# Kernel optimization log

Hardware: AMD Instinct MI355X
Metric: run time of the kernel (lower is better)

The kernel has to match this reference:

```python
import jax, jax.numpy as jnp
import numpy as np

N_NODES = 100000
N_EDGES = 3200000
IN_CH = 24
HIDDEN = 64
N_CLASSES = 16


def _sage_conv(x, src, dst, W_l, b_l, W_r, num_nodes):
    # mean-aggregate neighbor features at destination nodes
    msg = x[src]                                             # [E, F] gather
    agg = jax.ops.segment_sum(msg, dst, num_segments=num_nodes)
    deg = jax.ops.segment_sum(jnp.ones((src.shape[0],), x.dtype), dst,
                              num_segments=num_nodes)
    mean = agg / jnp.maximum(deg, 1.0)[:, None]
    # PyG SAGEConv: lin_l(aggregated) + lin_r(self); bias lives in lin_l
    return mean @ W_l.T + b_l + x @ W_r.T


def setup_inputs() -> dict:
    key = jax.random.key(0)
    ks = jax.random.split(key, 8)
    x = jax.random.normal(ks[0], (N_NODES, IN_CH), dtype=jnp.float32)
    edge_index = jax.random.randint(ks[1], (2, N_EDGES), 0, N_NODES, dtype=jnp.int64)
    s1 = 1.0 / np.sqrt(IN_CH)
    s2 = 1.0 / np.sqrt(HIDDEN)
    return {
        "x": x,
        "edge_index": edge_index,
        "W1_l": jax.random.normal(ks[2], (HIDDEN, IN_CH), dtype=jnp.float32) * s1,
        "b1": jnp.zeros((HIDDEN,), jnp.float32),
        "W1_r": jax.random.normal(ks[3], (HIDDEN, IN_CH), dtype=jnp.float32) * s1,
        "W2_l": jax.random.normal(ks[4], (HIDDEN, HIDDEN), dtype=jnp.float32) * s2,
        "b2": jnp.zeros((HIDDEN,), jnp.float32),
        "W2_r": jax.random.normal(ks[5], (HIDDEN, HIDDEN), dtype=jnp.float32) * s2,
        "Wc": jax.random.normal(ks[6], (N_CLASSES, HIDDEN), dtype=jnp.float32) * s2,
        "bc": jnp.zeros((N_CLASSES,), jnp.float32),
    }


def reference(x, edge_index, W1_l, b1, W1_r, W2_l, b2, W2_r, Wc, bc):
    num_nodes = x.shape[0]
    src, dst = edge_index[0], edge_index[1]
    h = _sage_conv(x, src, dst, W1_l, b1, W1_r, num_nodes)
    h = jax.nn.relu(h)
    # dropout is identity in eval mode
    embeddings = _sage_conv(h, src, dst, W2_l, b2, W2_r, num_nodes)
    logits = embeddings @ Wc.T + bc
    return (logits, embeddings)
```

## Files before the change

kernel.cpp:

```cpp
#include <hip/hip_runtime.h>

#define N_NODES 100000
#define N_EDGES 3200000
#define IN_CH 24
#define HIDDEN 64
#define N_CLASSES 16

#define NBUCK 782
#define CAP 4608
#define PTBLOCKS 256
#define PTCHUNK 12500
#define NSTRIPS (N_NODES / 16)

typedef __attribute__((ext_vector_type(8))) short short8;
typedef __attribute__((ext_vector_type(4))) float float4_;
typedef __attribute__((ext_vector_type(2))) float float2v;
typedef __attribute__((ext_vector_type(4))) int int4v;
typedef __attribute__((ext_vector_type(2))) unsigned uint2v;

__device__ unsigned llvm_amdgcn_raw_buffer_load_u32(int4v, int, int, int) __asm("llvm.amdgcn.raw.buffer.load.i32");
__device__ uint2v llvm_amdgcn_raw_buffer_load_u32x2(int4v, int, int, int) __asm("llvm.amdgcn.raw.buffer.load.v2i32");

__device__ __forceinline__ int4v make_srd(const void* p, unsigned bytes) {
    unsigned long long a = (unsigned long long)p;
    int4v r;
    r.x = (int)(unsigned)a;
    r.y = (int)((unsigned)(a >> 32) & 0xFFFFu);
    r.z = (int)bytes;
    r.w = 0x00020000;
    return r;
}

__device__ __forceinline__ unsigned short f2bf(float f) {
    union { float f; unsigned int u; } v; v.f = f;
    unsigned int u = v.u;
    return (unsigned short)((u + 0x7FFFu + ((u >> 16) & 1u)) >> 16);
}
__device__ __forceinline__ unsigned cvt_pk_bf16(float a, float b) {
    unsigned r;
    asm("v_cvt_pk_bf16_f32 %0, %1, %2" : "=v"(r) : "v"(a), "v"(b));
    return r;
}
__device__ __forceinline__ unsigned short pk_fp8(float a, float b) {
    return (unsigned short)(__builtin_amdgcn_cvt_pk_fp8_f32(a, b, 0, false) & 0xFFFF);
}
__device__ __forceinline__ void accum_dw(float2v* A, unsigned w) {
    A[0] += __builtin_amdgcn_cvt_pk_f32_fp8(w, false);
    A[1] += __builtin_amdgcn_cvt_pk_f32_fp8(w, true);
}


__global__ __launch_bounds__(256) void k_prep(const float* __restrict__ W1l,
                                              const float* __restrict__ W1r,
                                              const float* __restrict__ W2l,
                                              const float* __restrict__ W2r,
                                              const float* __restrict__ Wc,
                                              const float* __restrict__ b2,
                                              const float* __restrict__ bc,
                                              unsigned short* __restrict__ Bt1,
                                              unsigned short* __restrict__ Bt2,
                                              float* __restrict__ bias2,
                                              int* __restrict__ bucketFill) {
    int t = threadIdx.x;
    for (int i = t; i < NBUCK; i += 256) bucketFill[i] = 0;
    for (int i = t; i < 64 * 64; i += 256) {
        int o = i >> 6, k = i & 63;
        float v = (k < 24) ? W1r[o * 24 + k] : ((k < 48) ? W1l[o * 24 + k - 24] : 0.f);
        Bt1[i] = f2bf(v);
    }
    for (int i = t; i < 64 * 128; i += 256) {
        int o = i >> 7, k = i & 127;
        float v = (k < 64) ? W2l[o * 64 + k] : W2r[o * 64 + k - 64];
        Bt2[i] = f2bf(v);
    }
    for (int i = t; i < 16 * 128; i += 256) {
        int c = i >> 7, k = i & 127;
        const float* M = (k < 64) ? W2l : W2r;
        int kk = k & 63;
        float s = 0.f;
        for (int j = 0; j < 64; j++) s += Wc[c * 64 + j] * M[j * 64 + kk];
        Bt2[(64 + c) * 128 + k] = f2bf(s);
    }
    for (int i = t; i < 80; i += 256) {
        if (i < 64) bias2[i] = b2[i];
        else {
            int c = i - 64;
            float s = bc[c];
            for (int j = 0; j < 64; j++) s += Wc[c * 64 + j] * b2[j];
            bias2[i] = s;
        }
    }
}


__global__ __launch_bounds__(1024) void k_part(const int* __restrict__ src,
                                               const int* __restrict__ dst,
                                               int* __restrict__ bucketFill,
                                               unsigned int* __restrict__ pedges) {
    __shared__ int cntL[NBUCK];
    __shared__ int baseL[NBUCK];
    int t = threadIdx.x;
    int cbeg = blockIdx.x * PTCHUNK;
    int d[13], s[13];
#pragma unroll
    for (int k = 0; k < 13; k++) {
        int o = k * 1024 + t;
        bool ok = o < PTCHUNK;
        d[k] = ok ? dst[cbeg + o] : -1;
        s[k] = ok ? src[cbeg + o] : 0;
    }
    for (int i = t; i < NBUCK; i += 1024) cntL[i] = 0;
    __syncthreads();
#pragma unroll
    for (int k = 0; k < 13; k++)
        if (d[k] >= 0) atomicAdd(&cntL[d[k] >> 7], 1);
    __syncthreads();
    for (int i = t; i < NBUCK; i += 1024) {
        int c = cntL[i];
        if (c) baseL[i] = i * CAP + atomicAdd(&bucketFill[i], c);
        cntL[i] = 0;
    }
    __syncthreads();
#pragma unroll
    for (int k = 0; k < 13; k++)
        if (d[k] >= 0) {
            int bk = d[k] >> 7;
            int r = atomicAdd(&cntL[bk], 1);
            pedges[baseL[bk] + r] = ((unsigned int)(d[k] & 127) << 17) | (unsigned int)s[k];
        }
}

__global__ __launch_bounds__(1024) void k_bucket(const unsigned int* __restrict__ pedges,
                                                 const int* __restrict__ bucketFill,
                                                 int2* __restrict__ begend,
                                                 int* __restrict__ srcs, int N) {
    __shared__ int ncnt[128];
    __shared__ int sps[128];
    int b = blockIdx.x;
    int t = threadIdx.x;
    int eb0 = b * CAP;
    int m = bucketFill[b];
    unsigned int v[5];
#pragma unroll
    for (int k = 0; k < 5; k++) {
        int o = k * 1024 + t;
        v[k] = (o < m) ? pedges[eb0 + o] : 0xFFFFFFFFu;
    }
    if (t < 128) ncnt[t] = 0;
    __syncthreads();
#pragma unroll
    for (int k = 0; k < 5; k++)
        if (v[k] != 0xFFFFFFFFu) atomicAdd(&ncnt[v[k] >> 17], 1);
    __syncthreads();
    int myc = (t < 128) ? ncnt[t] : 0;
    int val = myc;
    if (t < 128) sps[t] = val;
    __syncthreads();
    for (int off = 1; off < 128; off <<= 1) {
        int vv = (t >= off && t < 128) ? sps[t - off] : 0;
        __syncthreads();
        if (t < 128) { val += vv; sps[t] = val; }
        __syncthreads();
    }
    int mybase = val - myc;
    int node = b * 128 + t;
    if (t < 128 && node < N) {
        int2 be; be.x = eb0 + mybase; be.y = eb0 + mybase + myc;
        begend[node] = be;
    }
    if (t < 128) { sps[t] = mybase; ncnt[t] = 0; }
    if (t < 32) srcs[eb0 + m + t] = 0;
    __syncthreads();
#pragma unroll
    for (int k = 0; k < 5; k++)
        if (v[k] != 0xFFFFFFFFu) {
            unsigned int nl = v[k] >> 17;
            int r = atomicAdd(&ncnt[nl], 1);
            srcs[eb0 + sps[nl] + r] = (int)(v[k] & 0x1FFFF);
        }
}

__global__ __launch_bounds__(256) void k_castx(const float* __restrict__ x,
                                               unsigned int* __restrict__ A1u,
                                               unsigned short* __restrict__ X8s) {
    int gid = blockIdx.x * 256 + threadIdx.x;
    if (gid >= N_NODES * 16) return;
    int n = gid >> 4, kp = gid & 15;
    if (kp < 12) {
        const float2 v = *(const float2*)(x + n * 24 + kp * 2);
        A1u[n * 32 + kp] = (unsigned int)f2bf(v.x) | ((unsigned int)f2bf(v.y) << 16);
        X8s[n * 16 + kp] = pk_fp8(v.x, v.y);
    } else {
        int p = kp - 12;
        uint2 z; z.x = 0u; z.y = 0u;
        *(uint2*)(A1u + n * 32 + 24 + p * 2) = z;
        X8s[n * 16 + kp] = 0;
    }
}


__global__ __launch_bounds__(256) void k_agg1(const unsigned int* __restrict__ X8u,
                                              const int2* __restrict__ begend,
                                              const int* __restrict__ srcs,
                                              unsigned int* __restrict__ A1w, int N) {
    int node = (blockIdx.x * 256 + threadIdx.x) >> 6;
    int lane = threadIdx.x & 63;
    if (node >= N) return;
    int2 be = begend[node];
    int b = be.x, e = be.y;
    int grp = lane >> 3;
    int sub = lane & 7;
    const int4v srdX = make_srd(X8u, N_NODES * 32u);
    const int4v srdS = make_srd(srcs, (unsigned)NBUCK * CAP * 4u);
    int suboff = sub * 4;
    float2v A[2] = {{0.f, 0.f}, {0.f, 0.f}};
    int nfull = (e - b) & ~31;
    int j = b;
    int vo = (b + grp) * 4;
    for (; j < b + nfull; j += 32, vo += 128) {
        int s0 = (int)llvm_amdgcn_raw_buffer_load_u32(srdS, vo, 0, 0);
        int s1 = (int)llvm_amdgcn_raw_buffer_load_u32(srdS, vo + 32, 0, 0);
        int s2 = (int)llvm_amdgcn_raw_buffer_load_u32(srdS, vo + 64, 0, 0);
        int s3 = (int)llvm_amdgcn_raw_buffer_load_u32(srdS, vo + 96, 0, 0);
        unsigned u0 = llvm_amdgcn_raw_buffer_load_u32(srdX, (s0 << 5) + suboff, 0, 0);
        unsigned u1 = llvm_amdgcn_raw_buffer_load_u32(srdX, (s1 << 5) + suboff, 0, 0);
        unsigned u2 = llvm_amdgcn_raw_buffer_load_u32(srdX, (s2 << 5) + suboff, 0, 0);
        unsigned u3 = llvm_amdgcn_raw_buffer_load_u32(srdX, (s3 << 5) + suboff, 0, 0);
        accum_dw(A, u0); accum_dw(A, u1); accum_dw(A, u2); accum_dw(A, u3);
    }
    if (j < e) {
        int j0 = j + grp;
        int s0 = (int)llvm_amdgcn_raw_buffer_load_u32(srdS, vo, 0, 0);
        int s1 = (int)llvm_amdgcn_raw_buffer_load_u32(srdS, vo + 32, 0, 0);
        int s2 = (int)llvm_amdgcn_raw_buffer_load_u32(srdS, vo + 64, 0, 0);
        int s3 = (int)llvm_amdgcn_raw_buffer_load_u32(srdS, vo + 96, 0, 0);
        int o0 = (j0 < e)      ? ((s0 << 5) + suboff) : 0x7FFF0000;
        int o1 = (j0 + 8 < e)  ? ((s1 << 5) + suboff) : 0x7FFF0000;
        int o2 = (j0 + 16 < e) ? ((s2 << 5) + suboff) : 0x7FFF0000;
        int o3 = (j0 + 24 < e) ? ((s3 << 5) + suboff) : 0x7FFF0000;
        unsigned u0 = llvm_amdgcn_raw_buffer_load_u32(srdX, o0, 0, 0);
        unsigned u1 = llvm_amdgcn_raw_buffer_load_u32(srdX, o1, 0, 0);
        unsigned u2 = llvm_amdgcn_raw_buffer_load_u32(srdX, o2, 0, 0);
        unsigned u3 = llvm_amdgcn_raw_buffer_load_u32(srdX, o3, 0, 0);
        accum_dw(A, u0); accum_dw(A, u1); accum_dw(A, u2); accum_dw(A, u3);
    }
#pragma unroll
    for (int mm = 8; mm <= 32; mm <<= 1) {
#pragma unroll
        for (int q = 0; q < 2; q++) {
            float2v t;
            t.x = __shfl_xor(A[q].x, mm, 64);
            t.y = __shfl_xor(A[q].y, mm, 64);
            A[q] += t;
        }
    }
    if (lane < 8) {
        float inv = __builtin_amdgcn_rcpf((float)max(e - b, 1));
        uint2v o;
        o.x = cvt_pk_bf16(A[0].x * inv, A[0].y * inv);
        o.y = cvt_pk_bf16(A[1].x * inv, A[1].y * inv);
        *(uint2v*)(A1w + (size_t)node * 32 + 12 + sub * 2) = o;
    }
}

__global__ __launch_bounds__(256) void k_agg2(const unsigned int* __restrict__ H8u,
                                              const int2* __restrict__ begend,
                                              const int* __restrict__ srcs,
                                              unsigned int* __restrict__ A2w, int N) {
    int node = (blockIdx.x * 256 + threadIdx.x) >> 6;
    int lane = threadIdx.x & 63;
    if (node >= N) return;
    int2 be = begend[node];
    int b = be.x, e = be.y;
    int grp = lane >> 3;
    int sub = lane & 7;
    const int4v srdH = make_srd(H8u, N_NODES * 64u);
    const int4v srdS = make_srd(srcs, (unsigned)NBUCK * CAP * 4u);
    int suboff = sub * 8;
    float2v A[4] = {{0.f, 0.f}, {0.f, 0.f}, {0.f, 0.f}, {0.f, 0.f}};
    int nfull = (e - b) & ~31;
    int j = b;
    int vo = (b + grp) * 4;
    for (; j < b + nfull; j += 32, vo += 128) {
        int s0 = (int)llvm_amdgcn_raw_buffer_load_u32(srdS, vo, 0, 0);
        int s1 = (int)llvm_amdgcn_raw_buffer_load_u32(srdS, vo + 32, 0, 0);
        int s2 = (int)llvm_amdgcn_raw_buffer_load_u32(srdS, vo + 64, 0, 0);
        int s3 = (int)llvm_amdgcn_raw_buffer_load_u32(srdS, vo + 96, 0, 0);
        uint2v u0 = llvm_amdgcn_raw_buffer_load_u32x2(srdH, (s0 << 6) + suboff, 0, 0);
        uint2v u1 = llvm_amdgcn_raw_buffer_load_u32x2(srdH, (s1 << 6) + suboff, 0, 0);
        uint2v u2 = llvm_amdgcn_raw_buffer_load_u32x2(srdH, (s2 << 6) + suboff, 0, 0);
        uint2v u3 = llvm_amdgcn_raw_buffer_load_u32x2(srdH, (s3 << 6) + suboff, 0, 0);
        accum_dw(A, u0.x); accum_dw(A + 2, u0.y);
        accum_dw(A, u1.x); accum_dw(A + 2, u1.y);
        accum_dw(A, u2.x); accum_dw(A + 2, u2.y);
        accum_dw(A, u3.x); accum_dw(A + 2, u3.y);
    }
    if (j < e) {
        int j0 = j + grp;
        int s0 = (int)llvm_amdgcn_raw_buffer_load_u32(srdS, vo, 0, 0);
        int s1 = (int)llvm_amdgcn_raw_buffer_load_u32(srdS, vo + 32, 0, 0);
        int s2 = (int)llvm_amdgcn_raw_buffer_load_u32(srdS, vo + 64, 0, 0);
        int s3 = (int)llvm_amdgcn_raw_buffer_load_u32(srdS, vo + 96, 0, 0);
        int o0 = (j0 < e)      ? ((s0 << 6) + suboff) : 0x7FFF0000;
        int o1 = (j0 + 8 < e)  ? ((s1 << 6) + suboff) : 0x7FFF0000;
        int o2 = (j0 + 16 < e) ? ((s2 << 6) + suboff) : 0x7FFF0000;
        int o3 = (j0 + 24 < e) ? ((s3 << 6) + suboff) : 0x7FFF0000;
        uint2v u0 = llvm_amdgcn_raw_buffer_load_u32x2(srdH, o0, 0, 0);
        uint2v u1 = llvm_amdgcn_raw_buffer_load_u32x2(srdH, o1, 0, 0);
        uint2v u2 = llvm_amdgcn_raw_buffer_load_u32x2(srdH, o2, 0, 0);
        uint2v u3 = llvm_amdgcn_raw_buffer_load_u32x2(srdH, o3, 0, 0);
        accum_dw(A, u0.x); accum_dw(A + 2, u0.y);
        accum_dw(A, u1.x); accum_dw(A + 2, u1.y);
        accum_dw(A, u2.x); accum_dw(A + 2, u2.y);
        accum_dw(A, u3.x); accum_dw(A + 2, u3.y);
    }
#pragma unroll
    for (int mm = 8; mm <= 32; mm <<= 1) {
#pragma unroll
        for (int q = 0; q < 4; q++) {
            float2v t;
            t.x = __shfl_xor(A[q].x, mm, 64);
            t.y = __shfl_xor(A[q].y, mm, 64);
            A[q] += t;
        }
    }
    if (lane < 8) {
        float inv = __builtin_amdgcn_rcpf((float)max(e - b, 1));
        uint4 o;
        o.x = cvt_pk_bf16(A[0].x * inv, A[0].y * inv);
        o.y = cvt_pk_bf16(A[1].x * inv, A[1].y * inv);
        o.z = cvt_pk_bf16(A[2].x * inv, A[2].y * inv);
        o.w = cvt_pk_bf16(A[3].x * inv, A[3].y * inv);
        *(uint4*)(A2w + (size_t)node * 64 + sub * 4) = o;
    }
}


__global__ __launch_bounds__(256) void k_gemm1(const unsigned short* __restrict__ A1,
                                               const unsigned short* __restrict__ Bt1,
                                               const float* __restrict__ b1,
                                               unsigned short* __restrict__ A2s,
                                               unsigned char* __restrict__ H8b) {
    int wave = (blockIdx.x * 256 + threadIdx.x) >> 6;
    int lane = threadIdx.x & 63;
    int m = lane & 15, quad = lane >> 4;
    if (wave >= NSTRIPS) return;
    short8 bf[4][2];
#pragma unroll
    for (int t = 0; t < 4; t++)
#pragma unroll
        for (int s = 0; s < 2; s++)
            bf[t][s] = *(const short8*)(Bt1 + (t * 16 + m) * 64 + s * 32 + quad * 8);
    float bias[4];
#pragma unroll
    for (int t = 0; t < 4; t++) bias[t] = b1[t * 16 + m];

    int row0 = wave * 16;
    short8 a0 = *(const short8*)(A1 + (row0 + m) * 64 + quad * 8);
    short8 a1 = *(const short8*)(A1 + (row0 + m) * 64 + 32 + quad * 8);
    float4_ acc[4];
#pragma unroll
    for (int t = 0; t < 4; t++) {
        float4_ c = {0.f, 0.f, 0.f, 0.f};
        c = __builtin_amdgcn_mfma_f32_16x16x32_bf16(a0, bf[t][0], c, 0, 0, 0);
        c = __builtin_amdgcn_mfma_f32_16x16x32_bf16(a1, bf[t][1], c, 0, 0, 0);
        acc[t] = c;
    }
#pragma unroll
    for (int t = 0; t < 4; t++) {
        int col = t * 16 + m;
#pragma unroll
        for (int r = 0; r < 4; r++) {
            int row = row0 + quad * 4 + r;
            float v = fmaxf(acc[t][r] + bias[t], 0.f);
            A2s[row * 128 + 64 + col] = f2bf(v);
            H8b[row * 64 + col] =
                (unsigned char)(__builtin_amdgcn_cvt_pk_fp8_f32(v, 0.f, 0, false) & 0xFF);
        }
    }
}

__global__ __launch_bounds__(256) void k_gemm2(const unsigned short* __restrict__ Bt2,
                                               const float* __restrict__ bias2,
                                               unsigned short* A2s,
                                               float* logits) {
    int wave = (blockIdx.x * 256 + threadIdx.x) >> 6;
    int lane = threadIdx.x & 63;
    int m = lane & 15, quad = lane >> 4;
    if (wave >= NSTRIPS) return;
    short8 bf[5][4];
#pragma unroll
    for (int t = 0; t < 5; t++)
#pragma unroll
        for (int s = 0; s < 4; s++)
            bf[t][s] = *(const short8*)(Bt2 + (t * 16 + m) * 128 + s * 32 + quad * 8);
    float bias[5];
#pragma unroll
    for (int t = 0; t < 5; t++) bias[t] = bias2[t * 16 + m];

    int row0 = wave * 16;
    short8 a[4];
#pragma unroll
    for (int s = 0; s < 4; s++)
        a[s] = *(const short8*)(A2s + (row0 + m) * 128 + s * 32 + quad * 8);
    float4_ acc[5];
#pragma unroll
    for (int t = 0; t < 5; t++) {
        float4_ c = {0.f, 0.f, 0.f, 0.f};
#pragma unroll
        for (int s = 0; s < 4; s++)
            c = __builtin_amdgcn_mfma_f32_16x16x32_bf16(a[s], bf[t][s], c, 0, 0, 0);
        acc[t] = c;
    }
    float* embp = (float*)A2s;
#pragma unroll
    for (int t = 0; t < 4; t++) {
#pragma unroll
        for (int r = 0; r < 4; r++) {
            int row = row0 + quad * 4 + r;
            embp[row * 64 + t * 16 + m] = acc[t][r] + bias[t];
        }
    }
#pragma unroll
    for (int r = 0; r < 4; r++) {
        int row = row0 + quad * 4 + r;
        logits[row * 16 + m] = acc[4][r] + bias[4];
    }
}


extern "C" void kernel_launch(void* const* d_in, const int* in_sizes, int n_in,
                              void* d_out, int out_size, void* d_ws, size_t ws_size,
                              hipStream_t stream) {
    const float* x = (const float*)d_in[0];
    const int* edge = (const int*)d_in[1];
    const int* srcIdx = edge;
    const int* dstIdx = edge + N_EDGES;
    const float* W1l = (const float*)d_in[2];
    const float* b1  = (const float*)d_in[3];
    const float* W1r = (const float*)d_in[4];
    const float* W2l = (const float*)d_in[5];
    const float* b2  = (const float*)d_in[6];
    const float* W2r = (const float*)d_in[7];
    const float* Wc  = (const float*)d_in[8];
    const float* bc  = (const float*)d_in[9];

    float* logits = (float*)d_out;
    unsigned short* A2s = (unsigned short*)((float*)d_out + (size_t)N_NODES * N_CLASSES);
    unsigned int* A2u = (unsigned int*)A2s;

    char* w = (char*)d_ws;
    auto carve = [&](size_t bytes) {
        char* p = w;
        w += (bytes + 255) & ~(size_t)255;
        return p;
    };
    int2* begend         = (int2*)carve((size_t)N_NODES * sizeof(int2));
    int* srcs            = (int*)carve((size_t)NBUCK * CAP * sizeof(int));
    unsigned int* A1u    = (unsigned int*)carve((size_t)N_NODES * 32 * sizeof(unsigned int));
    unsigned short* X8s  = (unsigned short*)carve((size_t)N_NODES * 32);
    unsigned char* H8b   = (unsigned char*)carve((size_t)N_NODES * 64);
    int* bucketFill      = (int*)carve(NBUCK * sizeof(int));
    unsigned short* Bt1  = (unsigned short*)carve(64 * 64 * sizeof(unsigned short));
    unsigned short* Bt2  = (unsigned short*)carve(80 * 128 * sizeof(unsigned short));
    float* bias2         = (float*)carve(80 * sizeof(float));

    unsigned int* pedges = (unsigned int*)A1u;
    unsigned short* A1s = (unsigned short*)A1u;
    unsigned int* X8u = (unsigned int*)X8s;
    unsigned int* H8u = (unsigned int*)H8b;

    k_prep<<<1, 256, 0, stream>>>(W1l, W1r, W2l, W2r, Wc, b2, bc, Bt1, Bt2, bias2,
                                  bucketFill);
    k_part<<<PTBLOCKS, 1024, 0, stream>>>(srcIdx, dstIdx, bucketFill, pedges);
    k_bucket<<<NBUCK, 1024, 0, stream>>>(pedges, bucketFill, begend, srcs, N_NODES);

    k_castx<<<(N_NODES * 16 + 255) / 256, 256, 0, stream>>>(x, A1u, X8s);
    int agrid = (N_NODES * 64 + 255) / 256;
    k_agg1<<<agrid, 256, 0, stream>>>(X8u, begend, srcs, A1u, N_NODES);
    k_gemm1<<<(NSTRIPS + 3) / 4, 256, 0, stream>>>(A1s, Bt1, b1, A2s, H8b);
    k_agg2<<<agrid, 256, 0, stream>>>(H8u, begend, srcs, A2u, N_NODES);
    k_gemm2<<<(NSTRIPS + 3) / 4, 256, 0, stream>>>(Bt2, bias2, A2s, logits);
}
```

Measured before the change: 278.2 us.

## Split layer-2 aggregation into two feature-half passes

Splits the second-layer neighbor aggregation into two kernel launches, each gathering only half of every 64-byte H row (32 bytes) per edge. The goal is a smaller gather working set per pass, so the half-feature table stays better resident in cache during random-source gathers. In exchange the edge index list and begin/end ranges are read twice, there is one extra launch, and each gather becomes a narrower 4-byte load.

```diff
diff --git a/kernel.cpp b/kernel.cpp
--- a/kernel.cpp
+++ b/kernel.cpp
@@ -263,10 +263,11 @@
     }
 }
 
-__global__ __launch_bounds__(256) void k_agg2(const unsigned int* __restrict__ H8u,
-                                              const int2* __restrict__ begend,
-                                              const int* __restrict__ srcs,
-                                              unsigned int* __restrict__ A2w, int N) {
+template <int HALF>
+__global__ __launch_bounds__(256) void k_agg2h(const unsigned int* __restrict__ H8u,
+                                               const int2* __restrict__ begend,
+                                               const int* __restrict__ srcs,
+                                               unsigned int* __restrict__ A2w, int N) {
     int node = (blockIdx.x * 256 + threadIdx.x) >> 6;
     int lane = threadIdx.x & 63;
     if (node >= N) return;
@@ -276,8 +277,8 @@
     int sub = lane & 7;
     const int4v srdH = make_srd(H8u, N_NODES * 64u);
     const int4v srdS = make_srd(srcs, (unsigned)NBUCK * CAP * 4u);
-    int suboff = sub * 8;
-    float2v A[4] = {{0.f, 0.f}, {0.f, 0.f}, {0.f, 0.f}, {0.f, 0.f}};
+    int suboff = HALF * 32 + sub * 4;
+    float2v A[2] = {{0.f, 0.f}, {0.f, 0.f}};
     int nfull = (e - b) & ~31;
     int j = b;
     int vo = (b + grp) * 4;
@@ -286,14 +287,11 @@
         int s1 = (int)llvm_amdgcn_raw_buffer_load_u32(srdS, vo + 32, 0, 0);
         int s2 = (int)llvm_amdgcn_raw_buffer_load_u32(srdS, vo + 64, 0, 0);
         int s3 = (int)llvm_amdgcn_raw_buffer_load_u32(srdS, vo + 96, 0, 0);
-        uint2v u0 = llvm_amdgcn_raw_buffer_load_u32x2(srdH, (s0 << 6) + suboff, 0, 0);
-        uint2v u1 = llvm_amdgcn_raw_buffer_load_u32x2(srdH, (s1 << 6) + suboff, 0, 0);
-        uint2v u2 = llvm_amdgcn_raw_buffer_load_u32x2(srdH, (s2 << 6) + suboff, 0, 0);
-        uint2v u3 = llvm_amdgcn_raw_buffer_load_u32x2(srdH, (s3 << 6) + suboff, 0, 0);
-        accum_dw(A, u0.x); accum_dw(A + 2, u0.y);
-        accum_dw(A, u1.x); accum_dw(A + 2, u1.y);
-        accum_dw(A, u2.x); accum_dw(A + 2, u2.y);
-        accum_dw(A, u3.x); accum_dw(A + 2, u3.y);
+        unsigned u0 = llvm_amdgcn_raw_buffer_load_u32(srdH, (s0 << 6) + suboff, 0, 0);
+        unsigned u1 = llvm_amdgcn_raw_buffer_load_u32(srdH, (s1 << 6) + suboff, 0, 0);
+        unsigned u2 = llvm_amdgcn_raw_buffer_load_u32(srdH, (s2 << 6) + suboff, 0, 0);
+        unsigned u3 = llvm_amdgcn_raw_buffer_load_u32(srdH, (s3 << 6) + suboff, 0, 0);
+        accum_dw(A, u0); accum_dw(A, u1); accum_dw(A, u2); accum_dw(A, u3);
     }
     if (j < e) {
         int j0 = j + grp;
@@ -305,19 +303,16 @@
         int o1 = (j0 + 8 < e)  ? ((s1 << 6) + suboff) : 0x7FFF0000;
         int o2 = (j0 + 16 < e) ? ((s2 << 6) + suboff) : 0x7FFF0000;
         int o3 = (j0 + 24 < e) ? ((s3 << 6) + suboff) : 0x7FFF0000;
-        uint2v u0 = llvm_amdgcn_raw_buffer_load_u32x2(srdH, o0, 0, 0);
-        uint2v u1 = llvm_amdgcn_raw_buffer_load_u32x2(srdH, o1, 0, 0);
-        uint2v u2 = llvm_amdgcn_raw_buffer_load_u32x2(srdH, o2, 0, 0);
-        uint2v u3 = llvm_amdgcn_raw_buffer_load_u32x2(srdH, o3, 0, 0);
-        accum_dw(A, u0.x); accum_dw(A + 2, u0.y);
-        accum_dw(A, u1.x); accum_dw(A + 2, u1.y);
-        accum_dw(A, u2.x); accum_dw(A + 2, u2.y);
-        accum_dw(A, u3.x); accum_dw(A + 2, u3.y);
+        unsigned u0 = llvm_amdgcn_raw_buffer_load_u32(srdH, o0, 0, 0);
+        unsigned u1 = llvm_amdgcn_raw_buffer_load_u32(srdH, o1, 0, 0);
+        unsigned u2 = llvm_amdgcn_raw_buffer_load_u32(srdH, o2, 0, 0);
+        unsigned u3 = llvm_amdgcn_raw_buffer_load_u32(srdH, o3, 0, 0);
+        accum_dw(A, u0); accum_dw(A, u1); accum_dw(A, u2); accum_dw(A, u3);
     }
 #pragma unroll
     for (int mm = 8; mm <= 32; mm <<= 1) {
 #pragma unroll
-        for (int q = 0; q < 4; q++) {
+        for (int q = 0; q < 2; q++) {
             float2v t;
             t.x = __shfl_xor(A[q].x, mm, 64);
             t.y = __shfl_xor(A[q].y, mm, 64);
@@ -326,12 +321,10 @@
     }
     if (lane < 8) {
         float inv = __builtin_amdgcn_rcpf((float)max(e - b, 1));
-        uint4 o;
+        uint2v o;
         o.x = cvt_pk_bf16(A[0].x * inv, A[0].y * inv);
         o.y = cvt_pk_bf16(A[1].x * inv, A[1].y * inv);
-        o.z = cvt_pk_bf16(A[2].x * inv, A[2].y * inv);
-        o.w = cvt_pk_bf16(A[3].x * inv, A[3].y * inv);
-        *(uint4*)(A2w + (size_t)node * 64 + sub * 4) = o;
+        *(uint2v*)(A2w + (size_t)node * 64 + HALF * 16 + sub * 2) = o;
     }
 }
 
@@ -479,6 +472,7 @@
     int agrid = (N_NODES * 64 + 255) / 256;
     k_agg1<<<agrid, 256, 0, stream>>>(X8u, begend, srcs, A1u, N_NODES);
     k_gemm1<<<(NSTRIPS + 3) / 4, 256, 0, stream>>>(A1s, Bt1, b1, A2s, H8b);
-    k_agg2<<<agrid, 256, 0, stream>>>(H8u, begend, srcs, A2u, N_NODES);
+    k_agg2h<0><<<agrid, 256, 0, stream>>>(H8u, begend, srcs, A2u, N_NODES);
+    k_agg2h<1><<<agrid, 256, 0, stream>>>(H8u, begend, srcs, A2u, N_NODES);
     k_gemm2<<<(NSTRIPS + 3) / 4, 256, 0, stream>>>(Bt2, bias2, A2s, logits);
 }
```

Result: slower. 304.2 us (+9.3%).

## Fuse neighbor aggregation with MFMA GEMM per 16-node tile in each layer

Applied to the files above, without the earlier changes.

Replaces the separate aggregate and GEMM kernels for both layers with fused kernels. Each block aggregates 16 nodes (4 per wave) into LDS and then runs the bf16 MFMA for that tile directly. Layer 1 now builds its self-feature operand straight from fp32 x, so the bf16 A1 staging buffer is no longer written or read, and k_castx only emits the fp8 copy. This removes global round trips of intermediates and two launches. In exchange each wave walks 4 nodes serially before the GEMM, which reduces gather parallelism per wave and adds a block barrier. The logits tile is computed only by wave 3, so that wave does extra work.

```diff
diff --git a/kernel.cpp b/kernel.cpp
--- a/kernel.cpp
+++ b/kernel.cpp
@@ -10,7 +10,6 @@
 #define CAP 4608
 #define PTBLOCKS 256
 #define PTCHUNK 12500
-#define NSTRIPS (N_NODES / 16)
 
 typedef __attribute__((ext_vector_type(8))) short short8;
 typedef __attribute__((ext_vector_type(4))) float float4_;
@@ -47,6 +46,11 @@
 __device__ __forceinline__ void accum_dw(float2v* A, unsigned w) {
     A[0] += __builtin_amdgcn_cvt_pk_f32_fp8(w, false);
     A[1] += __builtin_amdgcn_cvt_pk_f32_fp8(w, true);
+}
+__device__ __forceinline__ short8 mk8(unsigned d0, unsigned d1, unsigned d2, unsigned d3) {
+    union { unsigned u[4]; short8 s; } v;
+    v.u[0] = d0; v.u[1] = d1; v.u[2] = d2; v.u[3] = d3;
+    return v.s;
 }
 
 
@@ -181,250 +185,243 @@
 }
 
 __global__ __launch_bounds__(256) void k_castx(const float* __restrict__ x,
-                                               unsigned int* __restrict__ A1u,
                                                unsigned short* __restrict__ X8s) {
     int gid = blockIdx.x * 256 + threadIdx.x;
     if (gid >= N_NODES * 16) return;
     int n = gid >> 4, kp = gid & 15;
     if (kp < 12) {
         const float2 v = *(const float2*)(x + n * 24 + kp * 2);
-        A1u[n * 32 + kp] = (unsigned int)f2bf(v.x) | ((unsigned int)f2bf(v.y) << 16);
         X8s[n * 16 + kp] = pk_fp8(v.x, v.y);
     } else {
-        int p = kp - 12;
-        uint2 z; z.x = 0u; z.y = 0u;
-        *(uint2*)(A1u + n * 32 + 24 + p * 2) = z;
         X8s[n * 16 + kp] = 0;
     }
 }
 
 
-__global__ __launch_bounds__(256) void k_agg1(const unsigned int* __restrict__ X8u,
-                                              const int2* __restrict__ begend,
-                                              const int* __restrict__ srcs,
-                                              unsigned int* __restrict__ A1w, int N) {
-    int node = (blockIdx.x * 256 + threadIdx.x) >> 6;
+__global__ __launch_bounds__(256) void k_fuse1(const float* __restrict__ x,
+                                               const unsigned int* __restrict__ X8u,
+                                               const int2* __restrict__ begend,
+                                               const int* __restrict__ srcs,
+                                               const unsigned short* __restrict__ Bt1,
+                                               const float* __restrict__ b1,
+                                               unsigned short* __restrict__ A2s,
+                                               unsigned char* __restrict__ H8b) {
+    __shared__ unsigned int lds_mean[16][20];
+    int w = threadIdx.x >> 6;
     int lane = threadIdx.x & 63;
-    if (node >= N) return;
-    int2 be = begend[node];
-    int b = be.x, e = be.y;
+    int base = blockIdx.x * 16;
     int grp = lane >> 3;
     int sub = lane & 7;
     const int4v srdX = make_srd(X8u, N_NODES * 32u);
     const int4v srdS = make_srd(srcs, (unsigned)NBUCK * CAP * 4u);
     int suboff = sub * 4;
-    float2v A[2] = {{0.f, 0.f}, {0.f, 0.f}};
-    int nfull = (e - b) & ~31;
-    int j = b;
-    int vo = (b + grp) * 4;
-    for (; j < b + nfull; j += 32, vo += 128) {
-        int s0 = (int)llvm_amdgcn_raw_buffer_load_u32(srdS, vo, 0, 0);
-        int s1 = (int)llvm_amdgcn_raw_buffer_load_u32(srdS, vo + 32, 0, 0);
-        int s2 = (int)llvm_amdgcn_raw_buffer_load_u32(srdS, vo + 64, 0, 0);
-        int s3 = (int)llvm_amdgcn_raw_buffer_load_u32(srdS, vo + 96, 0, 0);
-        unsigned u0 = llvm_amdgcn_raw_buffer_load_u32(srdX, (s0 << 5) + suboff, 0, 0);
-        unsigned u1 = llvm_amdgcn_raw_buffer_load_u32(srdX, (s1 << 5) + suboff, 0, 0);
-        unsigned u2 = llvm_amdgcn_raw_buffer_load_u32(srdX, (s2 << 5) + suboff, 0, 0);
-        unsigned u3 = llvm_amdgcn_raw_buffer_load_u32(srdX, (s3 << 5) + suboff, 0, 0);
-        accum_dw(A, u0); accum_dw(A, u1); accum_dw(A, u2); accum_dw(A, u3);
-    }
-    if (j < e) {
-        int j0 = j + grp;
-        int s0 = (int)llvm_amdgcn_raw_buffer_load_u32(srdS, vo, 0, 0);
-        int s1 = (int)llvm_amdgcn_raw_buffer_load_u32(srdS, vo + 32, 0, 0);
-        int s2 = (int)llvm_amdgcn_raw_buffer_load_u32(srdS, vo + 64, 0, 0);
-        int s3 = (int)llvm_amdgcn_raw_buffer_load_u32(srdS, vo + 96, 0, 0);
-        int o0 = (j0 < e)      ? ((s0 << 5) + suboff) : 0x7FFF0000;
-        int o1 = (j0 + 8 < e)  ? ((s1 << 5) + suboff) : 0x7FFF0000;
-        int o2 = (j0 + 16 < e) ? ((s2 << 5) + suboff) : 0x7FFF0000;
-        int o3 = (j0 + 24 < e) ? ((s3 << 5) + suboff) : 0x7FFF0000;
-        unsigned u0 = llvm_amdgcn_raw_buffer_load_u32(srdX, o0, 0, 0);
-        unsigned u1 = llvm_amdgcn_raw_buffer_load_u32(srdX, o1, 0, 0);
-        unsigned u2 = llvm_amdgcn_raw_buffer_load_u32(srdX, o2, 0, 0);
-        unsigned u3 = llvm_amdgcn_raw_buffer_load_u32(srdX, o3, 0, 0);
-        accum_dw(A, u0); accum_dw(A, u1); accum_dw(A, u2); accum_dw(A, u3);
-    }
-#pragma unroll
-    for (int mm = 8; mm <= 32; mm <<= 1) {
-#pragma unroll
-        for (int q = 0; q < 2; q++) {
-            float2v t;
-            t.x = __shfl_xor(A[q].x, mm, 64);
-            t.y = __shfl_xor(A[q].y, mm, 64);
-            A[q] += t;
-        }
-    }
-    if (lane < 8) {
-        float inv = __builtin_amdgcn_rcpf((float)max(e - b, 1));
-        uint2v o;
-        o.x = cvt_pk_bf16(A[0].x * inv, A[0].y * inv);
-        o.y = cvt_pk_bf16(A[1].x * inv, A[1].y * inv);
-        *(uint2v*)(A1w + (size_t)node * 32 + 12 + sub * 2) = o;
-    }
-}
-
-__global__ __launch_bounds__(256) void k_agg2(const unsigned int* __restrict__ H8u,
-                                              const int2* __restrict__ begend,
-                                              const int* __restrict__ srcs,
-                                              unsigned int* __restrict__ A2w, int N) {
-    int node = (blockIdx.x * 256 + threadIdx.x) >> 6;
+
+    for (int i = 0; i < 4; i++) {
+        int il = w * 4 + i;
+        int2 be = begend[base + il];
+        int b = be.x, e = be.y;
+        float2v A[2] = {{0.f, 0.f}, {0.f, 0.f}};
+        int nfull = (e - b) & ~31;
+        int j = b;
+        int vo = (b + grp) * 4;
+        for (; j < b + nfull; j += 32, vo += 128) {
+            int s0 = (int)llvm_amdgcn_raw_buffer_load_u32(srdS, vo, 0, 0);
+            int s1 = (int)llvm_amdgcn_raw_buffer_load_u32(srdS, vo + 32, 0, 0);
+            int s2 = (int)llvm_amdgcn_raw_buffer_load_u32(srdS, vo + 64, 0, 0);
+            int s3 = (int)llvm_amdgcn_raw_buffer_load_u32(srdS, vo + 96, 0, 0);
+            unsigned u0 = llvm_amdgcn_raw_buffer_load_u32(srdX, (s0 << 5) + suboff, 0, 0);
+            unsigned u1 = llvm_amdgcn_raw_buffer_load_u32(srdX, (s1 << 5) + suboff, 0, 0);
+            unsigned u2 = llvm_amdgcn_raw_buffer_load_u32(srdX, (s2 << 5) + suboff, 0, 0);
+            unsigned u3 = llvm_amdgcn_raw_buffer_load_u32(srdX, (s3 << 5) + suboff, 0, 0);
+            accum_dw(A, u0); accum_dw(A, u1); accum_dw(A, u2); accum_dw(A, u3);
+        }
+        if (j < e) {
+            int j0 = j + grp;
+            int s0 = (int)llvm_amdgcn_raw_buffer_load_u32(srdS, vo, 0, 0);
+            int s1 = (int)llvm_amdgcn_raw_buffer_load_u32(srdS, vo + 32, 0, 0);
+            int s2 = (int)llvm_amdgcn_raw_buffer_load_u32(srdS, vo + 64, 0, 0);
+            int s3 = (int)llvm_amdgcn_raw_buffer_load_u32(srdS, vo + 96, 0, 0);
+            int o0 = (j0 < e)      ? ((s0 << 5) + suboff) : 0x7FFF0000;
+            int o1 = (j0 + 8 < e)  ? ((s1 << 5) + suboff) : 0x7FFF0000;
+            int o2 = (j0 + 16 < e) ? ((s2 << 5) + suboff) : 0x7FFF0000;
+            int o3 = (j0 + 24 < e) ? ((s3 << 5) + suboff) : 0x7FFF0000;
+            unsigned u0 = llvm_amdgcn_raw_buffer_load_u32(srdX, o0, 0, 0);
+            unsigned u1 = llvm_amdgcn_raw_buffer_load_u32(srdX, o1, 0, 0);
+            unsigned u2 = llvm_amdgcn_raw_buffer_load_u32(srdX, o2, 0, 0);
+            unsigned u3 = llvm_amdgcn_raw_buffer_load_u32(srdX, o3, 0, 0);
+            accum_dw(A, u0); accum_dw(A, u1); accum_dw(A, u2); accum_dw(A, u3);
+        }
+#pragma unroll
+        for (int mm = 8; mm <= 32; mm <<= 1) {
+#pragma unroll
+            for (int q = 0; q < 2; q++) {
+                float2v t;
+                t.x = __shfl_xor(A[q].x, mm, 64);
+                t.y = __shfl_xor(A[q].y, mm, 64);
+                A[q] += t;
+            }
+        }
+        if (lane < 8) {
+            float inv = __builtin_amdgcn_rcpf((float)max(e - b, 1));
+            lds_mean[il][sub * 2]     = cvt_pk_bf16(A[0].x * inv, A[0].y * inv);
+            lds_mean[il][sub * 2 + 1] = cvt_pk_bf16(A[1].x * inv, A[1].y * inv);
+        }
+    }
+    __syncthreads();
+
+    int m = lane & 15, quad = lane >> 4;
+    int row = base + m;
+    short8 bf0 = *(const short8*)(Bt1 + (w * 16 + m) * 64 + quad * 8);
+    short8 bf1 = *(const short8*)(Bt1 + (w * 16 + m) * 64 + 32 + quad * 8);
+    float bias = b1[w * 16 + m];
+    short8 a0, a1;
+    if (quad < 3) {
+        const float4* xp = (const float4*)(x + row * 24 + quad * 8);
+        float4 v0 = xp[0], v1 = xp[1];
+        a0 = mk8(cvt_pk_bf16(v0.x, v0.y), cvt_pk_bf16(v0.z, v0.w),
+                 cvt_pk_bf16(v1.x, v1.y), cvt_pk_bf16(v1.z, v1.w));
+    } else {
+        a0 = *(const short8*)&lds_mean[m][0];
+    }
+    if (quad == 0)      a1 = *(const short8*)&lds_mean[m][4];
+    else if (quad == 1) a1 = *(const short8*)&lds_mean[m][8];
+    else                a1 = mk8(0u, 0u, 0u, 0u);
+    float4_ c = {0.f, 0.f, 0.f, 0.f};
+    c = __builtin_amdgcn_mfma_f32_16x16x32_bf16(a0, bf0, c, 0, 0, 0);
+    c = __builtin_amdgcn_mfma_f32_16x16x32_bf16(a1, bf1, c, 0, 0, 0);
+    int col = w * 16 + m;
+#pragma unroll
+    for (int r = 0; r < 4; r++) {
+        int row2 = base + quad * 4 + r;
+        float v = fmaxf(c[r] + bias, 0.f);
+        A2s[row2 * 128 + 64 + col] = f2bf(v);
+        H8b[row2 * 64 + col] =
+            (unsigned char)(__builtin_amdgcn_cvt_pk_fp8_f32(v, 0.f, 0, false) & 0xFF);
+    }
+}
+
+__global__ __launch_bounds__(256) void k_fuse2(const unsigned int* __restrict__ H8u,
+                                               const int2* __restrict__ begend,
+                                               const int* __restrict__ srcs,
+                                               const unsigned short* __restrict__ Bt2,
+                                               const float* __restrict__ bias2,
+                                               unsigned short* A2s,
+                                               float* __restrict__ logits) {
+    __shared__ unsigned int lds_h[16][36];
+    int w = threadIdx.x >> 6;
     int lane = threadIdx.x & 63;
-    if (node >= N) return;
-    int2 be = begend[node];
-    int b = be.x, e = be.y;
+    int base = blockIdx.x * 16;
     int grp = lane >> 3;
     int sub = lane & 7;
     const int4v srdH = make_srd(H8u, N_NODES * 64u);
     const int4v srdS = make_srd(srcs, (unsigned)NBUCK * CAP * 4u);
     int suboff = sub * 8;
-    float2v A[4] = {{0.f, 0.f}, {0.f, 0.f}, {0.f, 0.f}, {0.f, 0.f}};
-    int nfull = (e - b) & ~31;
-    int j = b;
-    int vo = (b + grp) * 4;
-    for (; j < b + nfull; j += 32, vo += 128) {
-        int s0 = (int)llvm_amdgcn_raw_buffer_load_u32(srdS, vo, 0, 0);
-        int s1 = (int)llvm_amdgcn_raw_buffer_load_u32(srdS, vo + 32, 0, 0);
-        int s2 = (int)llvm_amdgcn_raw_buffer_load_u32(srdS, vo + 64, 0, 0);
-        int s3 = (int)llvm_amdgcn_raw_buffer_load_u32(srdS, vo + 96, 0, 0);
-        uint2v u0 = llvm_amdgcn_raw_buffer_load_u32x2(srdH, (s0 << 6) + suboff, 0, 0);
-        uint2v u1 = llvm_amdgcn_raw_buffer_load_u32x2(srdH, (s1 << 6) + suboff, 0, 0);
-        uint2v u2 = llvm_amdgcn_raw_buffer_load_u32x2(srdH, (s2 << 6) + suboff, 0, 0);
-        uint2v u3 = llvm_amdgcn_raw_buffer_load_u32x2(srdH, (s3 << 6) + suboff, 0, 0);
-        accum_dw(A, u0.x); accum_dw(A + 2, u0.y);
-        accum_dw(A, u1.x); accum_dw(A + 2, u1.y);
-        accum_dw(A, u2.x); accum_dw(A + 2, u2.y);
-        accum_dw(A, u3.x); accum_dw(A + 2, u3.y);
-    }
-    if (j < e) {
-        int j0 = j + grp;
-        int s0 = (int)llvm_amdgcn_raw_buffer_load_u32(srdS, vo, 0, 0);
-        int s1 = (int)llvm_amdgcn_raw_buffer_load_u32(srdS, vo + 32, 0, 0);
-        int s2 = (int)llvm_amdgcn_raw_buffer_load_u32(srdS, vo + 64, 0, 0);
-        int s3 = (int)llvm_amdgcn_raw_buffer_load_u32(srdS, vo + 96, 0, 0);
-        int o0 = (j0 < e)      ? ((s0 << 6) + suboff) : 0x7FFF0000;
-        int o1 = (j0 + 8 < e)  ? ((s1 << 6) + suboff) : 0x7FFF0000;
-        int o2 = (j0 + 16 < e) ? ((s2 << 6) + suboff) : 0x7FFF0000;
-        int o3 = (j0 + 24 < e) ? ((s3 << 6) + suboff) : 0x7FFF0000;
-        uint2v u0 = llvm_amdgcn_raw_buffer_load_u32x2(srdH, o0, 0, 0);
-        uint2v u1 = llvm_amdgcn_raw_buffer_load_u32x2(srdH, o1, 0, 0);
-        uint2v u2 = llvm_amdgcn_raw_buffer_load_u32x2(srdH, o2, 0, 0);
-        uint2v u3 = llvm_amdgcn_raw_buffer_load_u32x2(srdH, o3, 0, 0);
-        accum_dw(A, u0.x); accum_dw(A + 2, u0.y);
-        accum_dw(A, u1.x); accum_dw(A + 2, u1.y);
-        accum_dw(A, u2.x); accum_dw(A + 2, u2.y);
-        accum_dw(A, u3.x); accum_dw(A + 2, u3.y);
-    }
-#pragma unroll
-    for (int mm = 8; mm <= 32; mm <<= 1) {
-#pragma unroll
-        for (int q = 0; q < 4; q++) {
-            float2v t;
-            t.x = __shfl_xor(A[q].x, mm, 64);
-            t.y = __shfl_xor(A[q].y, mm, 64);
-            A[q] += t;
-        }
-    }
-    if (lane < 8) {
-        float inv = __builtin_amdgcn_rcpf((float)max(e - b, 1));
-        uint4 o;
-        o.x = cvt_pk_bf16(A[0].x * inv, A[0].y * inv);
-        o.y = cvt_pk_bf16(A[1].x * inv, A[1].y * inv);
-        o.z = cvt_pk_bf16(A[2].x * inv, A[2].y * inv);
-        o.w = cvt_pk_bf16(A[3].x * inv, A[3].y * inv);
-        *(uint4*)(A2w + (size_t)node * 64 + sub * 4) = o;
-    }
-}
-
-
-__global__ __launch_bounds__(256) void k_gemm1(const unsigned short* __restrict__ A1,
-                                               const unsigned short* __restrict__ Bt1,
-                                               const float* __restrict__ b1,
-                                               unsigned short* __restrict__ A2s,
-                                               unsigned char* __restrict__ H8b) {
-    int wave = (blockIdx.x * 256 + threadIdx.x) >> 6;
-    int lane = threadIdx.x & 63;
+
+    for (int i = 0; i < 4; i++) {
+        int il = w * 4 + i;
+        int2 be = begend[base + il];
+        int b = be.x, e = be.y;
+        float2v A[4] = {{0.f, 0.f}, {0.f, 0.f}, {0.f, 0.f}, {0.f, 0.f}};
+        int nfull = (e - b) & ~31;
+        int j = b;
+        int vo = (b + grp) * 4;
+        for (; j < b + nfull; j += 32, vo += 128) {
+            int s0 = (int)llvm_amdgcn_raw_buffer_load_u32(srdS, vo, 0, 0);
+            int s1 = (int)llvm_amdgcn_raw_buffer_load_u32(srdS, vo + 32, 0, 0);
+            int s2 = (int)llvm_amdgcn_raw_buffer_load_u32(srdS, vo + 64, 0, 0);
+            int s3 = (int)llvm_amdgcn_raw_buffer_load_u32(srdS, vo + 96, 0, 0);
+            uint2v u0 = llvm_amdgcn_raw_buffer_load_u32x2(srdH, (s0 << 6) + suboff, 0, 0);
+            uint2v u1 = llvm_amdgcn_raw_buffer_load_u32x2(srdH, (s1 << 6) + suboff, 0, 0);
+            uint2v u2 = llvm_amdgcn_raw_buffer_load_u32x2(srdH, (s2 << 6) + suboff, 0, 0);
+            uint2v u3 = llvm_amdgcn_raw_buffer_load_u32x2(srdH, (s3 << 6) + suboff, 0, 0);
+            accum_dw(A, u0.x); accum_dw(A + 2, u0.y);
+            accum_dw(A, u1.x); accum_dw(A + 2, u1.y);
+            accum_dw(A, u2.x); accum_dw(A + 2, u2.y);
+            accum_dw(A, u3.x); accum_dw(A + 2, u3.y);
+        }
+        if (j < e) {
+            int j0 = j + grp;
+            int s0 = (int)llvm_amdgcn_raw_buffer_load_u32(srdS, vo, 0, 0);
+            int s1 = (int)llvm_amdgcn_raw_buffer_load_u32(srdS, vo + 32, 0, 0);
+            int s2 = (int)llvm_amdgcn_raw_buffer_load_u32(srdS, vo + 64, 0, 0);
+            int s3 = (int)llvm_amdgcn_raw_buffer_load_u32(srdS, vo + 96, 0, 0);
+            int o0 = (j0 < e)      ? ((s0 << 6) + suboff) : 0x7FFF0000;
+            int o1 = (j0 + 8 < e)  ? ((s1 << 6) + suboff) : 0x7FFF0000;
+            int o2 = (j0 + 16 < e) ? ((s2 << 6) + suboff) : 0x7FFF0000;
+            int o3 = (j0 + 24 < e) ? ((s3 << 6) + suboff) : 0x7FFF0000;
+            uint2v u0 = llvm_amdgcn_raw_buffer_load_u32x2(srdH, o0, 0, 0);
+            uint2v u1 = llvm_amdgcn_raw_buffer_load_u32x2(srdH, o1, 0, 0);
+            uint2v u2 = llvm_amdgcn_raw_buffer_load_u32x2(srdH, o2, 0, 0);
+            uint2v u3 = llvm_amdgcn_raw_buffer_load_u32x2(srdH, o3, 0, 0);
+            accum_dw(A, u0.x); accum_dw(A + 2, u0.y);
+            accum_dw(A, u1.x); accum_dw(A + 2, u1.y);
+            accum_dw(A, u2.x); accum_dw(A + 2, u2.y);
+            accum_dw(A, u3.x); accum_dw(A + 2, u3.y);
+        }
+#pragma unroll
+        for (int mm = 8; mm <= 32; mm <<= 1) {
+#pragma unroll
+            for (int q = 0; q < 4; q++) {
+                float2v t;
+                t.x = __shfl_xor(A[q].x, mm, 64);
+                t.y = __shfl_xor(A[q].y, mm, 64);
+                A[q] += t;
+            }
+        }
+        if (lane < 8) {
+            float inv = __builtin_amdgcn_rcpf((float)max(e - b, 1));
+            uint4 o;
+            o.x = cvt_pk_bf16(A[0].x * inv, A[0].y * inv);
+            o.y = cvt_pk_bf16(A[1].x * inv, A[1].y * inv);
+            o.z = cvt_pk_bf16(A[2].x * inv, A[2].y * inv);
+            o.w = cvt_pk_bf16(A[3].x * inv, A[3].y * inv);
+            *(uint4*)&lds_h[il][sub * 4] = o;
+        }
+    }
+    __syncthreads();
+
     int m = lane & 15, quad = lane >> 4;
-    if (wave >= NSTRIPS) return;
-    short8 bf[4][2];
-#pragma unroll
-    for (int t = 0; t < 4; t++)
-#pragma unroll
-        for (int s = 0; s < 2; s++)
-            bf[t][s] = *(const short8*)(Bt1 + (t * 16 + m) * 64 + s * 32 + quad * 8);
-    float bias[4];
-#pragma unroll
-    for (int t = 0; t < 4; t++) bias[t] = b1[t * 16 + m];
-
-    int row0 = wave * 16;
-    short8 a0 = *(const short8*)(A1 + (row0 + m) * 64 + quad * 8);
-    short8 a1 = *(const short8*)(A1 + (row0 + m) * 64 + 32 + quad * 8);
-    float4_ acc[4];
-#pragma unroll
-    for (int t = 0; t < 4; t++) {
-        float4_ c = {0.f, 0.f, 0.f, 0.f};
-        c = __builtin_amdgcn_mfma_f32_16x16x32_bf16(a0, bf[t][0], c, 0, 0, 0);
-        c = __builtin_amdgcn_mfma_f32_16x16x32_bf16(a1, bf[t][1], c, 0, 0, 0);
-        acc[t] = c;
-    }
-#pragma unroll
-    for (int t = 0; t < 4; t++) {
-        int col = t * 16 + m;
+    int row = base + m;
+    short8 a0 = *(const short8*)&lds_h[m][quad * 4];
+    short8 a1 = *(const short8*)&lds_h[m][16 + quad * 4];
+    short8 a2 = *(const short8*)(A2s + row * 128 + 64 + quad * 8);
+    short8 a3 = *(const short8*)(A2s + row * 128 + 96 + quad * 8);
+    short8 bf[4], bg[4];
+#pragma unroll
+    for (int s = 0; s < 4; s++)
+        bf[s] = *(const short8*)(Bt2 + (w * 16 + m) * 128 + s * 32 + quad * 8);
+    float bias = bias2[w * 16 + m];
+    float bias4 = 0.f;
+    if (w == 3) {
+#pragma unroll
+        for (int s = 0; s < 4; s++)
+            bg[s] = *(const short8*)(Bt2 + (64 + m) * 128 + s * 32 + quad * 8);
+        bias4 = bias2[64 + m];
+    }
+    __syncthreads();
+    float4_ c = {0.f, 0.f, 0.f, 0.f};
+    c = __builtin_amdgcn_mfma_f32_16x16x32_bf16(a0, bf[0], c, 0, 0, 0);
+    c = __builtin_amdgcn_mfma_f32_16x16x32_bf16(a1, bf[1], c, 0, 0, 0);
+    c = __builtin_amdgcn_mfma_f32_16x16x32_bf16(a2, bf[2], c, 0, 0, 0);
+    c = __builtin_amdgcn_mfma_f32_16x16x32_bf16(a3, bf[3], c, 0, 0, 0);
+    float* embp = (float*)A2s;
+    int col = w * 16 + m;
+#pragma unroll
+    for (int r = 0; r < 4; r++) {
+        int row2 = base + quad * 4 + r;
+        embp[row2 * 64 + col] = c[r] + bias;
+    }
+    if (w == 3) {
+        float4_ cl = {0.f, 0.f, 0.f, 0.f};
+        cl = __builtin_amdgcn_mfma_f32_16x16x32_bf16(a0, bg[0], cl, 0, 0, 0);
+        cl = __builtin_amdgcn_mfma_f32_16x16x32_bf16(a1, bg[1], cl, 0, 0, 0);
+        cl = __builtin_amdgcn_mfma_f32_16x16x32_bf16(a2, bg[2], cl, 0, 0, 0);
+        cl = __builtin_amdgcn_mfma_f32_16x16x32_bf16(a3, bg[3], cl, 0, 0, 0);
 #pragma unroll
         for (int r = 0; r < 4; r++) {
-            int row = row0 + quad * 4 + r;
-            float v = fmaxf(acc[t][r] + bias[t], 0.f);
-            A2s[row * 128 + 64 + col] = f2bf(v);
-            H8b[row * 64 + col] =
-                (unsigned char)(__builtin_amdgcn_cvt_pk_fp8_f32(v, 0.f, 0, false) & 0xFF);
-        }
-    }
-}
-
-__global__ __launch_bounds__(256) void k_gemm2(const unsigned short* __restrict__ Bt2,
-                                               const float* __restrict__ bias2,
-                                               unsigned short* A2s,
-                                               float* logits) {
-    int wave = (blockIdx.x * 256 + threadIdx.x) >> 6;
-    int lane = threadIdx.x & 63;
-    int m = lane & 15, quad = lane >> 4;
-    if (wave >= NSTRIPS) return;
-    short8 bf[5][4];
-#pragma unroll
-    for (int t = 0; t < 5; t++)
-#pragma unroll
-        for (int s = 0; s < 4; s++)
-            bf[t][s] = *(const short8*)(Bt2 + (t * 16 + m) * 128 + s * 32 + quad * 8);
-    float bias[5];
-#pragma unroll
-    for (int t = 0; t < 5; t++) bias[t] = bias2[t * 16 + m];
-
-    int row0 = wave * 16;
-    short8 a[4];
-#pragma unroll
-    for (int s = 0; s < 4; s++)
-        a[s] = *(const short8*)(A2s + (row0 + m) * 128 + s * 32 + quad * 8);
-    float4_ acc[5];
-#pragma unroll
-    for (int t = 0; t < 5; t++) {
-        float4_ c = {0.f, 0.f, 0.f, 0.f};
-#pragma unroll
-        for (int s = 0; s < 4; s++)
-            c = __builtin_amdgcn_mfma_f32_16x16x32_bf16(a[s], bf[t][s], c, 0, 0, 0);
-        acc[t] = c;
-    }
-    float* embp = (float*)A2s;
-#pragma unroll
-    for (int t = 0; t < 4; t++) {
-#pragma unroll
-        for (int r = 0; r < 4; r++) {
-            int row = row0 + quad * 4 + r;
-            embp[row * 64 + t * 16 + m] = acc[t][r] + bias[t];
-        }
-    }
-#pragma unroll
-    for (int r = 0; r < 4; r++) {
-        int row = row0 + quad * 4 + r;
-        logits[row * 16 + m] = acc[4][r] + bias[4];
+            int row2 = base + quad * 4 + r;
+            logits[row2 * 16 + m] = cl[r] + bias4;
+        }
     }
 }
 
@@ -447,7 +444,6 @@
 
     float* logits = (float*)d_out;
     unsigned short* A2s = (unsigned short*)((float*)d_out + (size_t)N_NODES * N_CLASSES);
-    unsigned int* A2u = (unsigned int*)A2s;
 
     char* w = (char*)d_ws;
     auto carve = [&](size_t bytes) {
@@ -457,7 +453,7 @@
     };
     int2* begend         = (int2*)carve((size_t)N_NODES * sizeof(int2));
     int* srcs            = (int*)carve((size_t)NBUCK * CAP * sizeof(int));
-    unsigned int* A1u    = (unsigned int*)carve((size_t)N_NODES * 32 * sizeof(unsigned int));
+    unsigned int* pedges = (unsigned int*)carve((size_t)NBUCK * CAP * sizeof(unsigned int));
     unsigned short* X8s  = (unsigned short*)carve((size_t)N_NODES * 32);
     unsigned char* H8b   = (unsigned char*)carve((size_t)N_NODES * 64);
     int* bucketFill      = (int*)carve(NBUCK * sizeof(int));
@@ -465,8 +461,6 @@
     unsigned short* Bt2  = (unsigned short*)carve(80 * 128 * sizeof(unsigned short));
     float* bias2         = (float*)carve(80 * sizeof(float));
 
-    unsigned int* pedges = (unsigned int*)A1u;
-    unsigned short* A1s = (unsigned short*)A1u;
     unsigned int* X8u = (unsigned int*)X8s;
     unsigned int* H8u = (unsigned int*)H8b;
 
@@ -474,11 +468,9 @@
                                   bucketFill);
     k_part<<<PTBLOCKS, 1024, 0, stream>>>(srcIdx, dstIdx, bucketFill, pedges);
     k_bucket<<<NBUCK, 1024, 0, stream>>>(pedges, bucketFill, begend, srcs, N_NODES);
-
-    k_castx<<<(N_NODES * 16 + 255) / 256, 256, 0, stream>>>(x, A1u, X8s);
-    int agrid = (N_NODES * 64 + 255) / 256;
-    k_agg1<<<agrid, 256, 0, stream>>>(X8u, begend, srcs, A1u, N_NODES);
-    k_gemm1<<<(NSTRIPS + 3) / 4, 256, 0, stream>>>(A1s, Bt1, b1, A2s, H8b);
-    k_agg2<<<agrid, 256, 0, stream>>>(H8u, begend, srcs, A2u, N_NODES);
-    k_gemm2<<<(NSTRIPS + 3) / 4, 256, 0, stream>>>(Bt2, bias2, A2s, logits);
-}
+    k_castx<<<(N_NODES * 16 + 255) / 256, 256, 0, stream>>>(x, X8s);
+
+    int fgrid = N_NODES / 16;
+    k_fuse1<<<fgrid, 256, 0, stream>>>(x, X8u, begend, srcs, Bt1, b1, A2s, H8b);
+    k_fuse2<<<fgrid, 256, 0, stream>>>(H8u, begend, srcs, Bt2, bias2, A2s, logits);
+}
```

After: 264.4 us. 5.0% less time.
